# Optimization experiments

Hardware: AMD Instinct MI355X
Metric: run time of the kernel (lower is better)

## Reference

```python
import jax, jax.numpy as jnp
import numpy as np

B, N_NUC, N_UP, N_DOWN = 512, 16, 32, 32
N_ELEC = N_UP + N_DOWN            # 64 electrons
F = 8                             # edge feature dim (Gaussian RBF envelopes)
D = N_NUC * F                     # embedding_dim = 128 (positional electron embeddings)
L = 3                             # n_interactions
N_ATOM_TYPES = 4


def _rbf(diff):
    # diff: [..., 3] -> [..., F]; Gaussian RBF features of the interparticle distance
    d = jnp.sqrt(jnp.sum(diff * diff, axis=-1) + 1e-12)
    mu = jnp.linspace(0.0, 4.0, F, dtype=diff.dtype)
    return jnp.exp(-(d[..., None] - mu) ** 2)


def setup_inputs() -> dict:
    key = jax.random.key(0)
    ks = jax.random.split(key, 9)
    r = 2.0 * jax.random.normal(ks[0], (B, N_ELEC, 3), dtype=jnp.float32)
    R = 2.0 * jax.random.normal(ks[1], (B, N_NUC, 3), dtype=jnp.float32)
    atom_types = jax.random.randint(ks[2], (N_NUC,), 0, N_ATOM_TYPES)
    embed_table = 0.1 * jax.random.normal(ks[3], (N_ATOM_TYPES, D), dtype=jnp.float32)
    we_same = 0.1 * jax.random.normal(ks[4], (L, F, D), dtype=jnp.float32)
    we_anti = 0.1 * jax.random.normal(ks[5], (L, F, D), dtype=jnp.float32)
    we_ne = 0.1 * jax.random.normal(ks[6], (L, F, D), dtype=jnp.float32)
    w_up = 0.05 * jax.random.normal(ks[7], (L, 4 * D, D), dtype=jnp.float32)
    b_up = jnp.zeros((L, D), dtype=jnp.float32)
    return {
        'r': r, 'R': R, 'embed_table': embed_table,
        'we_same': we_same, 'we_anti': we_anti, 'we_ne': we_ne,
        'w_up': w_up, 'b_up': b_up, 'atom_types': atom_types,
    }


def reference(r, R, embed_table, we_same, we_anti, we_ne, w_up, b_up, atom_types):
    # --- molecular graph edge construction (pairwise differences + edge features) ---
    ee_feat = _rbf(r[:, :, None, :] - r[:, None, :, :])   # [B, e, e, F]
    ne_feat = _rbf(r[:, :, None, :] - R[:, None, :, :])   # [B, e, n, F]

    spin = jnp.arange(N_ELEC) >= N_UP
    eye = jnp.eye(N_ELEC, dtype=bool)
    same_m = ((spin[:, None] == spin[None, :]) & ~eye).astype(ee_feat.dtype)  # no self-interaction
    anti_m = (spin[:, None] != spin[None, :]).astype(ee_feat.dtype)
    feat_same = ee_feat * same_m[None, :, :, None]
    feat_anti = ee_feat * anti_m[None, :, :, None]

    # --- node factory: positional electron embeddings (dense scatter of ne features == reshape) ---
    x = ne_feat.reshape(ne_feat.shape[0], N_ELEC, N_NUC * F)  # [B, e, D]
    y = embed_table[atom_types]                               # [n, D] nuclei embeddings

    # --- message-passing layers ---
    for l in range(L):
        # messages = Linear(edge_feats) * sender embedding, summed over senders per receiver;
        # contract sender axis first to keep intermediates at [B, e, F, D]
        t_s = jnp.einsum('bijf,bjd->bifd', feat_same, x)
        z_s = jnp.einsum('bifd,fd->bid', t_s, we_same[l])
        t_a = jnp.einsum('bijf,bjd->bifd', feat_anti, x)
        z_a = jnp.einsum('bifd,fd->bid', t_a, we_anti[l])
        t_n = jnp.einsum('binf,nd->bifd', ne_feat, y)
        z_n = jnp.einsum('bifd,fd->bid', t_n, we_ne[l])
        upd = jnp.concatenate([x, z_s, z_a, z_n], axis=-1)    # [B, e, 4D]
        x = x + jnp.tanh(upd @ w_up[l] + b_up[l])
    return x  # final electron embeddings [B, N_ELEC, D]
```

## Files before the change

### kernel.cpp

```cpp
#include <hip/hip_runtime.h>


typedef unsigned short u16;
typedef unsigned int u32;
typedef __attribute__((ext_vector_type(8))) short short8;
typedef __attribute__((ext_vector_type(4))) float f32x4;
typedef __attribute__((ext_vector_type(4))) u32 u32x4;
typedef _Float16 h2 __attribute__((ext_vector_type(2)));

__device__ __forceinline__ u16 f2h(float f){ return __builtin_bit_cast(u16, (_Float16)f); }
__device__ __forceinline__ float h2f(u16 a){ return (float)__builtin_bit_cast(_Float16, a); }

__device__ __forceinline__ short8 rbf8(float dd){
  short8 a;
#pragma unroll
  for (int f = 0; f < 8; f++){
    float u = dd - (4.0f/7.0f)*(float)f;
    a[f] = (short)f2h(__expf(-u*u));
  }
  return a;
}

__global__ __launch_bounds__(256) void gnn_prep(
    const float* __restrict__ w_up, const float* __restrict__ we_ne,
    const float* __restrict__ embed, const int* __restrict__ atypes,
    u16* __restrict__ wsegs){
  __shared__ u16 lw[16384];
  const int blk = blockIdx.x;
  const int l = blk / 5, seg = blk % 5;
  const int tid = threadIdx.x;
  if (seg < 4){
    const float* src = w_up + (l*512 + seg*128)*128;
#pragma unroll
    for (int mm = 0; mm < 16; mm++){
      int idx = mm*1024 + tid*4;
      float4 v = *(const float4*)(src + idx);
      lw[idx+0] = f2h(v.x); lw[idx+1] = f2h(v.y);
      lw[idx+2] = f2h(v.z); lw[idx+3] = f2h(v.w);
    }
  } else {
#pragma unroll
    for (int mm = 0; mm < 16; mm++){
      int idx = mm*1024 + tid*4;
      int k = idx >> 7, dout = idx & 127;
      int n = k >> 3, f = k & 7;
      float4 ye = *(const float4*)(embed + atypes[n]*128 + dout);
      float4 wn = *(const float4*)(we_ne + (l*8 + f)*128 + dout);
      lw[idx+0] = f2h(ye.x*wn.x); lw[idx+1] = f2h(ye.y*wn.y);
      lw[idx+2] = f2h(ye.z*wn.z); lw[idx+3] = f2h(ye.w*wn.w);
    }
  }
  __syncthreads();
  u16* dst = wsegs + blk*16384;
  const int col = tid & 15, q = (tid >> 4) & 3;
#pragma unroll
  for (int m = 0; m < 8; m++){
    int slot = m*4 + (tid >> 6);
    int c = slot >> 3, nt = slot & 7;
    int kbase = c*32 + q*8;
    int dout = nt*16 + col;
    short8 vv;
#pragma unroll
    for (int jj = 0; jj < 8; jj++) vv[jj] = (short)lw[(kbase+jj)*128 + dout];
    *(short8*)(dst + m*2048 + tid*8) = vv;
  }
}

__global__ __launch_bounds__(256, 2) void gnn_main(
    const float* __restrict__ r_g, const float* __restrict__ R_g,
    const float* __restrict__ weS_g, const float* __restrict__ weA_g,
    const float* __restrict__ bup_g,
    const u16* __restrict__ wsegs,
    float* __restrict__ out)
{
  extern __shared__ __attribute__((aligned(16))) u16 lds[];
  u16* const xb   = lds;
  u16* const zst1 = lds + 8704;
  u16* const zst2 = lds + 17408;
  float* const rs = (float*)(lds + 26112);
  float* const Rs = rs + 256;
  u32* const weP  = (u32*)(lds + 26752);

  const int tid  = threadIdx.x;
  const int lane = tid & 63;
  const int w    = tid >> 6;
  const int b    = blockIdx.x;
  const int col  = lane & 15;
  const int q    = lane >> 4;
  const int i0   = w * 16;
  const int sp   = w >> 1;
  const int mrow = i0 + col;
  const int loff = (q*16 + col) * 8;

  auto gemm_seg = [&](const u16* wseg_g, const u16* arows, f32x4* acc){
#pragma unroll
    for (int c = 0; c < 4; c++){
      short8 a = *(const short8*)(arows + mrow*136 + c*32 + (q<<3));
#pragma unroll
      for (int nt = 0; nt < 8; nt++){
        short8 bf = *(const short8*)(wseg_g + c*4096 + nt*512 + loff);
        acc[nt] = __builtin_amdgcn_mfma_f32_16x16x32_f16(a, bf, acc[nt], 0, 0, 0);
      }
    }
  };

  float px0, px1, px2;
  float dN[4];
  {
    if (tid < 64){
#pragma unroll
      for (int k = 0; k < 3; k++) rs[tid*4+k] = r_g[(b*64+tid)*3 + k];
    } else if (tid < 80){
      int n = tid - 64;
#pragma unroll
      for (int k = 0; k < 3; k++) Rs[n*4+k] = R_g[(b*16+n)*3 + k];
    }
#pragma unroll
    for (int e0 = 0; e0 < 3072; e0 += 256){
      int e = e0 + tid;
      int d = e & 127, p = (e >> 7) & 3, ps = (e >> 9) & 1, ll = e >> 10;
      const float* src = ps ? weA_g : weS_g;
      h2 t;
      t[0] = (_Float16)src[(ll*8 + 2*p  )*128 + d];
      t[1] = (_Float16)src[(ll*8 + 2*p+1)*128 + d];
      weP[((ll*2+ps)*4 + p)*128 + d] = __builtin_bit_cast(u32, t);
    }
    __syncthreads();
    px0 = rs[mrow*4]; px1 = rs[mrow*4+1]; px2 = rs[mrow*4+2];
#pragma unroll
    for (int c = 0; c < 4; c++){
      int n = 4*c + q;
      float dx = px0-Rs[n*4], dy = px1-Rs[n*4+1], dz = px2-Rs[n*4+2];
      dN[c] = sqrtf(dx*dx + dy*dy + dz*dz + 1e-12f);
    }
    {
      int i = tid >> 2, nb = (tid & 3)*4;
      float y0 = rs[i*4], y1 = rs[i*4+1], y2 = rs[i*4+2];
#pragma unroll
      for (int nn = 0; nn < 4; nn++){
        int n = nb + nn;
        float dx = y0-Rs[n*4], dy = y1-Rs[n*4+1], dz = y2-Rs[n*4+2];
        float dd = sqrtf(dx*dx + dy*dy + dz*dz + 1e-12f);
        *(short8*)&xb[i*136 + n*8] = rbf8(dd);
      }
    }
    __syncthreads();
  }

  f32x4 xr[8];
#pragma unroll
  for (int nt = 0; nt < 8; nt++)
#pragma unroll
    for (int rr = 0; rr < 4; rr++)
      xr[nt][rr] = h2f(xb[(i0 + q*4 + rr)*136 + nt*16 + col]);

  const f32x4 vzero = {0.f, 0.f, 0.f, 0.f};

#pragma unroll 1
  for (int l = 0; l < 3; l++){
    const u16* slab = wsegs + l*81920;

    f32x4 upd[8];
#pragma unroll
    for (int nt = 0; nt < 8; nt++) upd[nt] = vzero;

    auto zpass = [&](int pass, u16* zdst){
      const int jb0 = pass ? 32*(1-sp) : 32*sp;
      const u32* wbase = weP + ((l*2 + pass)*4)*128;
      h2 wpA[8][4];
#pragma unroll
      for (int nt = 0; nt < 8; nt++)
#pragma unroll
        for (int p = 0; p < 4; p++)
          wpA[nt][p] = __builtin_bit_cast(h2, wbase[p*128 + nt*16 + col]);
      f32x4 zacc[8];
#pragma unroll
      for (int nt = 0; nt < 8; nt++) zacc[nt] = vzero;
#pragma unroll
      for (int c = 0; c < 8; c++){
        int j = jb0 + 4*c + q;
        float dx = px0-rs[j*4], dy = px1-rs[j*4+1], dz = px2-rs[j*4+2];
        float dd = sqrtf(dx*dx + dy*dy + dz*dz + 1e-12f);
        short8 a = rbf8(dd);
        if (pass == 0 && j == mrow) a = (short8)0;
#pragma unroll
        for (int nt = 0; nt < 8; nt++){
          u16 xvv = xb[j*136 + nt*16 + col];
          _Float16 xh = __builtin_bit_cast(_Float16, xvv);
          h2 xd; xd[0] = xh; xd[1] = xh;
          u32x4 bu;
#pragma unroll
          for (int p = 0; p < 4; p++)
            bu[p] = __builtin_bit_cast(u32, (h2)(xd * wpA[nt][p]));
          short8 bf = __builtin_bit_cast(short8, bu);
          zacc[nt] = __builtin_amdgcn_mfma_f32_16x16x32_f16(a, bf, zacc[nt], 0, 0, 0);
        }
      }
#pragma unroll
      for (int nt = 0; nt < 8; nt++)
#pragma unroll
        for (int rr = 0; rr < 4; rr++)
          zdst[(i0 + q*4 + rr)*136 + nt*16 + col] = f2h(zacc[nt][rr]);
    };

    zpass(0, zst1);
    zpass(1, zst2);

    gemm_seg(slab + 0*16384, xb,   upd);
    gemm_seg(slab + 1*16384, zst1, upd);
    {
      const u16* yseg = slab + 4*16384;
      f32x4 zn[8];
#pragma unroll
      for (int nt = 0; nt < 8; nt++) zn[nt] = vzero;
#pragma unroll
      for (int c = 0; c < 4; c++){
        short8 a = rbf8(dN[c]);
#pragma unroll
        for (int nt = 0; nt < 8; nt++){
          short8 bf = *(const short8*)(yseg + c*4096 + nt*512 + loff);
          zn[nt] = __builtin_amdgcn_mfma_f32_16x16x32_f16(a, bf, zn[nt], 0, 0, 0);
        }
      }
#pragma unroll
      for (int nt = 0; nt < 8; nt++)
#pragma unroll
        for (int rr = 0; rr < 4; rr++)
          zst1[(i0 + q*4 + rr)*136 + nt*16 + col] = f2h(zn[nt][rr]);
    }
    gemm_seg(slab + 2*16384, zst2, upd);
    gemm_seg(slab + 3*16384, zst1, upd);

    {
      float bupr[8];
#pragma unroll
      for (int nt = 0; nt < 8; nt++) bupr[nt] = bup_g[l*128 + nt*16 + col];
#pragma unroll
      for (int nt = 0; nt < 8; nt++){
#pragma unroll
        for (int rr = 0; rr < 4; rr++){
          float v = upd[nt][rr] + bupr[nt];
          float e = __expf(2.0f * v);
          float th = 1.0f - 2.0f * __builtin_amdgcn_rcpf(e + 1.0f);
          xr[nt][rr] += th;
        }
      }
    }
    if (l < 2){
#pragma unroll
      for (int nt = 0; nt < 8; nt++)
#pragma unroll
        for (int rr = 0; rr < 4; rr++)
          xb[(i0 + q*4 + rr)*136 + nt*16 + col] = f2h(xr[nt][rr]);
      __syncthreads();
    } else {
#pragma unroll
      for (int nt = 0; nt < 8; nt++)
#pragma unroll
        for (int rr = 0; rr < 4; rr++)
          out[(b*64 + i0 + q*4 + rr)*128 + nt*16 + col] = xr[nt][rr];
    }
  }
}

extern "C" void kernel_launch(void* const* d_in, const int* in_sizes, int n_in,
                              void* d_out, int out_size, void* d_ws, size_t ws_size,
                              hipStream_t stream){
  const float* r     = (const float*)d_in[0];
  const float* R     = (const float*)d_in[1];
  const float* embed = (const float*)d_in[2];
  const float* weS   = (const float*)d_in[3];
  const float* weA   = (const float*)d_in[4];
  const float* weN   = (const float*)d_in[5];
  const float* wup   = (const float*)d_in[6];
  const float* bup   = (const float*)d_in[7];
  const int* atyp    = (const int*)d_in[8];

  u16* wsegs = (u16*)d_ws;

  (void)hipFuncSetAttribute((const void*)gnn_main,
                            hipFuncAttributeMaxDynamicSharedMemorySize, 65792);
  gnn_prep<<<15, 256, 0, stream>>>(wup, weN, embed, atyp, wsegs);
  gnn_main<<<512, 256, 65792, stream>>>(r, R, weS, weA, bup, wsegs, (float*)d_out);
}
```

Measured before the change: 146.2 us.

## Split each block's layer work across two wave halves with LDS partial-sum exchange

Doubles the block to 512 threads. One half computes the same-spin messages plus the x and z_same GEMM segments; the other computes the anti-spin and nuclear messages plus their segments. Partial update sums are exchanged through LDS before the tanh residual. The electron-pair RBF operands are computed once before the layer loop and kept in registers, and the message loop is reordered to load x per column tile. The residual x now lives only in fp16 in LDS instead of fp32 registers, which adds rounding error, and the tighter register budget at 512 threads risks spills.

```diff
diff --git a/kernel.cpp b/kernel.cpp
--- a/kernel.cpp
+++ b/kernel.cpp
@@ -66,7 +66,7 @@
   }
 }
 
-__global__ __launch_bounds__(256, 2) void gnn_main(
+__global__ __launch_bounds__(512, 2) void gnn_main(
     const float* __restrict__ r_g, const float* __restrict__ R_g,
     const float* __restrict__ weS_g, const float* __restrict__ weA_g,
     const float* __restrict__ bup_g,
@@ -75,20 +75,24 @@
 {
   extern __shared__ __attribute__((aligned(16))) u16 lds[];
   u16* const xb   = lds;
-  u16* const zst1 = lds + 8704;
-  u16* const zst2 = lds + 17408;
+  u16* const zstA = lds + 8704;
+  u16* const zstB = lds + 17408;
   float* const rs = (float*)(lds + 26112);
   float* const Rs = rs + 256;
   u32* const weP  = (u32*)(lds + 26752);
+  float* const exA = (float*)zstA;
+  float* const exB = (float*)zstB;
 
   const int tid  = threadIdx.x;
   const int lane = tid & 63;
   const int w    = tid >> 6;
+  const int half = w >> 2;
+  const int wq   = w & 3;
   const int b    = blockIdx.x;
   const int col  = lane & 15;
   const int q    = lane >> 4;
-  const int i0   = w * 16;
-  const int sp   = w >> 1;
+  const int i0   = wq * 16;
+  const int sp   = wq >> 1;
   const int mrow = i0 + col;
   const int loff = (q*16 + col) * 8;
 
@@ -104,8 +108,9 @@
     }
   };
 
+  short8 aC[8];
+  float dN[4];
   float px0, px1, px2;
-  float dN[4];
   {
     if (tid < 64){
 #pragma unroll
@@ -116,7 +121,7 @@
       for (int k = 0; k < 3; k++) Rs[n*4+k] = R_g[(b*16+n)*3 + k];
     }
 #pragma unroll
-    for (int e0 = 0; e0 < 3072; e0 += 256){
+    for (int e0 = 0; e0 < 3072; e0 += 512){
       int e = e0 + tid;
       int d = e & 127, p = (e >> 7) & 3, ps = (e >> 9) & 1, ll = e >> 10;
       const float* src = ps ? weA_g : weS_g;
@@ -127,17 +132,33 @@
     }
     __syncthreads();
     px0 = rs[mrow*4]; px1 = rs[mrow*4+1]; px2 = rs[mrow*4+2];
-#pragma unroll
-    for (int c = 0; c < 4; c++){
-      int n = 4*c + q;
-      float dx = px0-Rs[n*4], dy = px1-Rs[n*4+1], dz = px2-Rs[n*4+2];
-      dN[c] = sqrtf(dx*dx + dy*dy + dz*dz + 1e-12f);
+    if (half == 0){
+#pragma unroll
+      for (int c = 0; c < 8; c++){
+        int j = 32*sp + 4*c + q;
+        float dx = px0-rs[j*4], dy = px1-rs[j*4+1], dz = px2-rs[j*4+2];
+        aC[c] = rbf8(sqrtf(dx*dx + dy*dy + dz*dz + 1e-12f));
+        if (j == mrow) aC[c] = (short8)0;
+      }
+    } else {
+#pragma unroll
+      for (int c = 0; c < 8; c++){
+        int j = 32*(1-sp) + 4*c + q;
+        float dx = px0-rs[j*4], dy = px1-rs[j*4+1], dz = px2-rs[j*4+2];
+        aC[c] = rbf8(sqrtf(dx*dx + dy*dy + dz*dz + 1e-12f));
+      }
+#pragma unroll
+      for (int c = 0; c < 4; c++){
+        int n = 4*c + q;
+        float dx = px0-Rs[n*4], dy = px1-Rs[n*4+1], dz = px2-Rs[n*4+2];
+        dN[c] = sqrtf(dx*dx + dy*dy + dz*dz + 1e-12f);
+      }
     }
     {
-      int i = tid >> 2, nb = (tid & 3)*4;
+      int i = tid >> 3, nb = (tid & 7)*2;
       float y0 = rs[i*4], y1 = rs[i*4+1], y2 = rs[i*4+2];
 #pragma unroll
-      for (int nn = 0; nn < 4; nn++){
+      for (int nn = 0; nn < 2; nn++){
         int n = nb + nn;
         float dx = y0-Rs[n*4], dy = y1-Rs[n*4+1], dz = y2-Rs[n*4+2];
         float dd = sqrtf(dx*dx + dy*dy + dz*dz + 1e-12f);
@@ -147,13 +168,6 @@
     __syncthreads();
   }
 
-  f32x4 xr[8];
-#pragma unroll
-  for (int nt = 0; nt < 8; nt++)
-#pragma unroll
-    for (int rr = 0; rr < 4; rr++)
-      xr[nt][rr] = h2f(xb[(i0 + q*4 + rr)*136 + nt*16 + col]);
-
   const f32x4 vzero = {0.f, 0.f, 0.f, 0.f};
 
 #pragma unroll 1
@@ -167,33 +181,28 @@
     auto zpass = [&](int pass, u16* zdst){
       const int jb0 = pass ? 32*(1-sp) : 32*sp;
       const u32* wbase = weP + ((l*2 + pass)*4)*128;
-      h2 wpA[8][4];
-#pragma unroll
-      for (int nt = 0; nt < 8; nt++)
+      f32x4 zacc[8];
+#pragma unroll
+      for (int nt = 0; nt < 8; nt++) zacc[nt] = vzero;
+#pragma unroll
+      for (int nt = 0; nt < 8; nt++){
+        h2 wp[4];
 #pragma unroll
         for (int p = 0; p < 4; p++)
-          wpA[nt][p] = __builtin_bit_cast(h2, wbase[p*128 + nt*16 + col]);
-      f32x4 zacc[8];
-#pragma unroll
-      for (int nt = 0; nt < 8; nt++) zacc[nt] = vzero;
-#pragma unroll
-      for (int c = 0; c < 8; c++){
-        int j = jb0 + 4*c + q;
-        float dx = px0-rs[j*4], dy = px1-rs[j*4+1], dz = px2-rs[j*4+2];
-        float dd = sqrtf(dx*dx + dy*dy + dz*dz + 1e-12f);
-        short8 a = rbf8(dd);
-        if (pass == 0 && j == mrow) a = (short8)0;
-#pragma unroll
-        for (int nt = 0; nt < 8; nt++){
-          u16 xvv = xb[j*136 + nt*16 + col];
-          _Float16 xh = __builtin_bit_cast(_Float16, xvv);
+          wp[p] = __builtin_bit_cast(h2, wbase[p*128 + nt*16 + col]);
+        u16 xv[8];
+#pragma unroll
+        for (int c = 0; c < 8; c++) xv[c] = xb[(jb0 + 4*c + q)*136 + nt*16 + col];
+#pragma unroll
+        for (int c = 0; c < 8; c++){
+          _Float16 xh = __builtin_bit_cast(_Float16, xv[c]);
           h2 xd; xd[0] = xh; xd[1] = xh;
           u32x4 bu;
 #pragma unroll
           for (int p = 0; p < 4; p++)
-            bu[p] = __builtin_bit_cast(u32, (h2)(xd * wpA[nt][p]));
+            bu[p] = __builtin_bit_cast(u32, (h2)(xd * wp[p]));
           short8 bf = __builtin_bit_cast(short8, bu);
-          zacc[nt] = __builtin_amdgcn_mfma_f32_16x16x32_f16(a, bf, zacc[nt], 0, 0, 0);
+          zacc[nt] = __builtin_amdgcn_mfma_f32_16x16x32_f16(aC[c], bf, zacc[nt], 0, 0, 0);
         }
       }
 #pragma unroll
@@ -203,63 +212,65 @@
           zdst[(i0 + q*4 + rr)*136 + nt*16 + col] = f2h(zacc[nt][rr]);
     };
 
-    zpass(0, zst1);
-    zpass(1, zst2);
-
-    gemm_seg(slab + 0*16384, xb,   upd);
-    gemm_seg(slab + 1*16384, zst1, upd);
+    if (half == 0){
+      zpass(0, zstA);
+      gemm_seg(slab + 0*16384, xb,   upd);
+      gemm_seg(slab + 1*16384, zstA, upd);
+    } else {
+      zpass(1, zstB);
+      gemm_seg(slab + 2*16384, zstB, upd);
+      {
+        const u16* yseg = slab + 4*16384;
+        f32x4 zn[8];
+#pragma unroll
+        for (int nt = 0; nt < 8; nt++) zn[nt] = vzero;
+#pragma unroll
+        for (int c = 0; c < 4; c++){
+          short8 a = rbf8(dN[c]);
+#pragma unroll
+          for (int nt = 0; nt < 8; nt++){
+            short8 bf = *(const short8*)(yseg + c*4096 + nt*512 + loff);
+            zn[nt] = __builtin_amdgcn_mfma_f32_16x16x32_f16(a, bf, zn[nt], 0, 0, 0);
+          }
+        }
+#pragma unroll
+        for (int nt = 0; nt < 8; nt++)
+#pragma unroll
+          for (int rr = 0; rr < 4; rr++)
+            zstB[(i0 + q*4 + rr)*136 + nt*16 + col] = f2h(zn[nt][rr]);
+      }
+      gemm_seg(slab + 3*16384, zstB, upd);
+    }
+
     {
-      const u16* yseg = slab + 4*16384;
-      f32x4 zn[8];
-#pragma unroll
-      for (int nt = 0; nt < 8; nt++) zn[nt] = vzero;
-#pragma unroll
-      for (int c = 0; c < 4; c++){
-        short8 a = rbf8(dN[c]);
-#pragma unroll
-        for (int nt = 0; nt < 8; nt++){
-          short8 bf = *(const short8*)(yseg + c*4096 + nt*512 + loff);
-          zn[nt] = __builtin_amdgcn_mfma_f32_16x16x32_f16(a, bf, zn[nt], 0, 0, 0);
-        }
-      }
-#pragma unroll
-      for (int nt = 0; nt < 8; nt++)
+      float* exsend = half ? exB : exA;
+      const int ntoff = half ? 0 : 4;
+#pragma unroll
+      for (int nt = 0; nt < 4; nt++)
 #pragma unroll
         for (int rr = 0; rr < 4; rr++)
-          zst1[(i0 + q*4 + rr)*136 + nt*16 + col] = f2h(zn[nt][rr]);
-    }
-    gemm_seg(slab + 2*16384, zst2, upd);
-    gemm_seg(slab + 3*16384, zst1, upd);
-
+          exsend[(i0 + q*4 + rr)*68 + nt*16 + col] = upd[ntoff+nt][rr];
+    }
+    __syncthreads();
     {
-      float bupr[8];
-#pragma unroll
-      for (int nt = 0; nt < 8; nt++) bupr[nt] = bup_g[l*128 + nt*16 + col];
-#pragma unroll
-      for (int nt = 0; nt < 8; nt++){
+      const float* exrecv = half ? exA : exB;
+      const int ntk = half ? 4 : 0;
+#pragma unroll
+      for (int nt = 0; nt < 4; nt++){
+        float bupr = bup_g[l*128 + (ntk+nt)*16 + col];
 #pragma unroll
         for (int rr = 0; rr < 4; rr++){
-          float v = upd[nt][rr] + bupr[nt];
+          int row = i0 + q*4 + rr;
+          float v = upd[ntk+nt][rr] + exrecv[row*68 + nt*16 + col] + bupr;
           float e = __expf(2.0f * v);
           float th = 1.0f - 2.0f * __builtin_amdgcn_rcpf(e + 1.0f);
-          xr[nt][rr] += th;
+          float xn = h2f(xb[row*136 + (ntk+nt)*16 + col]) + th;
+          if (l < 2) xb[row*136 + (ntk+nt)*16 + col] = f2h(xn);
+          else       out[(b*64 + row)*128 + (ntk+nt)*16 + col] = xn;
         }
       }
     }
-    if (l < 2){
-#pragma unroll
-      for (int nt = 0; nt < 8; nt++)
-#pragma unroll
-        for (int rr = 0; rr < 4; rr++)
-          xb[(i0 + q*4 + rr)*136 + nt*16 + col] = f2h(xr[nt][rr]);
-      __syncthreads();
-    } else {
-#pragma unroll
-      for (int nt = 0; nt < 8; nt++)
-#pragma unroll
-        for (int rr = 0; rr < 4; rr++)
-          out[(b*64 + i0 + q*4 + rr)*128 + nt*16 + col] = xr[nt][rr];
-    }
+    if (l < 2) __syncthreads();
   }
 }
 
@@ -281,5 +292,5 @@
   (void)hipFuncSetAttribute((const void*)gnn_main,
                             hipFuncAttributeMaxDynamicSharedMemorySize, 65792);
   gnn_prep<<<15, 256, 0, stream>>>(wup, weN, embed, atyp, wsegs);
-  gnn_main<<<512, 256, 65792, stream>>>(r, R, weS, weA, bup, wsegs, (float*)d_out);
-}
+  gnn_main<<<512, 512, 65792, stream>>>(r, R, weS, weA, bup, wsegs, (float*)d_out);
+}
```

New measurement: 204.4 us. +39.8%, slower.
